# Optimization experiments

Measured on AMD Instinct MI355X. Metric: run time of the kernel, lower is better.

The kernel has to match this reference:

```python
import jax, jax.numpy as jnp
import numpy as np

HIDDEN = 1024
HEADS = 16
HEAD_DIM = HIDDEN // HEADS
FF = 4 * HIDDEN
B, S = 2, 2048


def _linear_params(key, out_dim, in_dim):
    kw, kb = jax.random.split(key)
    bound = 1.0 / np.sqrt(in_dim)
    W = jax.random.uniform(kw, (out_dim, in_dim), jnp.float32, -bound, bound)
    b = jax.random.uniform(kb, (out_dim,), jnp.float32, -bound, bound)
    return W, b


def setup_inputs() -> dict:
    key = jax.random.key(0)
    ks = jax.random.split(key, 8)
    x = jax.random.normal(ks[0], (B, S, HIDDEN), jnp.float32)
    attention_mask = jnp.ones((B, S), jnp.float32)
    Wq, bq = _linear_params(ks[1], HIDDEN, HIDDEN)
    Wk, bk = _linear_params(ks[2], HIDDEN, HIDDEN)
    Wv, bv = _linear_params(ks[3], HIDDEN, HIDDEN)
    Wo, bo = _linear_params(ks[4], HIDDEN, HIDDEN)
    W1, b1 = _linear_params(ks[5], FF, HIDDEN)
    W2, b2 = _linear_params(ks[6], HIDDEN, FF)
    g1 = jnp.ones((HIDDEN,), jnp.float32); be1 = jnp.zeros((HIDDEN,), jnp.float32)
    g2 = jnp.ones((HIDDEN,), jnp.float32); be2 = jnp.zeros((HIDDEN,), jnp.float32)
    return dict(x=x, attention_mask=attention_mask,
                Wq=Wq, bq=bq, Wk=Wk, bk=bk, Wv=Wv, bv=bv, Wo=Wo, bo=bo,
                W1=W1, b1=b1, W2=W2, b2=b2,
                g1=g1, be1=be1, g2=g2, be2=be2)


def _layer_norm(x, g, b, eps=1e-5):
    mu = jnp.mean(x, axis=-1, keepdims=True)
    var = jnp.mean(jnp.square(x - mu), axis=-1, keepdims=True)
    return (x - mu) * jax.lax.rsqrt(var + eps) * g + b


def reference(x, attention_mask, Wq, bq, Wk, bk, Wv, bv, Wo, bo,
              W1, b1, W2, b2, g1, be1, g2, be2):
    # Dropout is identity (eval mode / deterministic reference).
    residual = x
    h = _layer_norm(x, g1, be1)
    # [B,S,H] -> [B,nH,S,dh]
    def heads(t):
        return t.reshape(B, S, HEADS, HEAD_DIM).transpose(0, 2, 1, 3)
    q = heads(h @ Wq.T + bq)
    k = heads(h @ Wk.T + bk)
    v = heads(h @ Wv.T + bv)
    scores = jnp.einsum('bhqd,bhkd->bhqk', q, k) / np.sqrt(HEAD_DIM).astype(np.float32)
    scores = scores + (attention_mask[:, None, None, :] - 1.0) * 10000.0
    attn = jax.nn.softmax(scores, axis=-1)
    ctx = jnp.einsum('bhqk,bhkd->bhqd', attn, v)
    ctx = ctx.transpose(0, 2, 1, 3).reshape(B, S, HIDDEN)
    attn_out = ctx @ Wo.T + bo
    x = residual + attn_out
    residual = x
    h = _layer_norm(x, g2, be2)
    h = jax.nn.gelu(h @ W1.T + b1, approximate=False)
    h = h @ W2.T + b2
    return residual + h
```

## Files before the change

kernel.cpp:

```cpp
#include <hip/hip_runtime.h>
#include <hip/hip_bf16.h>
#include <math.h>

typedef __bf16 bf16;
typedef __bf16 bf16x4v __attribute__((ext_vector_type(4)));
typedef __bf16 bf16x8 __attribute__((ext_vector_type(8)));
typedef float  f32x4  __attribute__((ext_vector_type(4)));

#define HIDDEN 1024
#define TOKENS 4096
#define FFDIM  4096
#define SEQ    2048
#define NHEAD  16

#define LOG2E 1.44269504088896340736f

__device__ __forceinline__ void async_copy16(bf16* lds, const bf16* g)
{
    __builtin_amdgcn_global_load_lds(
        (__attribute__((address_space(1))) void*)g,
        (__attribute__((address_space(3))) void*)lds,
        16, 0, 0);
}

__global__ __launch_bounds__(256) void cvt_kernel(const float* __restrict__ in,
                                                  bf16* __restrict__ out, int n)
{
    int i = (blockIdx.x * 256 + threadIdx.x) * 4;
    if (i >= n) return;
    float4 v = *(const float4*)&in[i];
    bf16x4v o = { (bf16)v.x, (bf16)v.y, (bf16)v.z, (bf16)v.w };
    *(bf16x4v*)&out[i] = o;
}

__global__ __launch_bounds__(256) void cvt4_kernel(const float* __restrict__ s0,
    const float* __restrict__ s1, const float* __restrict__ s2, const float* __restrict__ s3,
    bf16* __restrict__ out)
{
    const int M1 = 1 << 20;
    int i = (blockIdx.x * 256 + threadIdx.x) * 4;
    int sel = i >> 20;
    const float* src = (sel == 0) ? s0 : (sel == 1) ? s1 : (sel == 2) ? s2 : s3;
    float4 v = *(const float4*)&src[i & (M1 - 1)];
    bf16x4v o = { (bf16)v.x, (bf16)v.y, (bf16)v.z, (bf16)v.w };
    *(bf16x4v*)&out[i] = o;
}

__global__ __launch_bounds__(256) void concat_bias_kernel(const float* __restrict__ bq,
    const float* __restrict__ bk, const float* __restrict__ bv, float* __restrict__ o)
{
    int i = blockIdx.x * 256 + threadIdx.x;
    float v = (i < 1024) ? bq[i] : (i < 2048 ? bk[i - 1024] : bv[i - 2048]);
    o[i] = v;
}

__global__ __launch_bounds__(256) void ln_kernel(const float* __restrict__ in,
    const float* __restrict__ g, const float* __restrict__ be, bf16* __restrict__ out)
{
    int row = blockIdx.x;
    int tid = threadIdx.x;
    const float* x = in + (size_t)row * HIDDEN;
    int i0 = tid * 4;
    float4 v = *(const float4*)&x[i0];
    float s  = v.x + v.y + v.z + v.w;
    float s2 = v.x*v.x + v.y*v.y + v.z*v.z + v.w*v.w;
    #pragma unroll
    for (int off = 32; off > 0; off >>= 1) { s += __shfl_xor(s, off); s2 += __shfl_xor(s2, off); }
    __shared__ float red[2][4];
    int wave = tid >> 6;
    if ((tid & 63) == 0) { red[0][wave] = s; red[1][wave] = s2; }
    __syncthreads();
    float ts  = red[0][0] + red[0][1] + red[0][2] + red[0][3];
    float ts2 = red[1][0] + red[1][1] + red[1][2] + red[1][3];
    float mu   = ts  * (1.0f / HIDDEN);
    float var  = ts2 * (1.0f / HIDDEN) - mu * mu;
    float rstd = rsqrtf(var + 1e-5f);
    float4 gg = *(const float4*)&g[i0];
    float4 bb = *(const float4*)&be[i0];
    bf16x4v o;
    o[0] = (bf16)((v.x - mu) * rstd * gg.x + bb.x);
    o[1] = (bf16)((v.y - mu) * rstd * gg.y + bb.y);
    o[2] = (bf16)((v.z - mu) * rstd * gg.z + bb.z);
    o[3] = (bf16)((v.w - mu) * rstd * gg.w + bb.w);
    *(bf16x4v*)&out[(size_t)row * HIDDEN + i0] = o;
}

template<int BM, int EPI, typename OT>
__global__ __launch_bounds__(256) void gemm_bt(const bf16* __restrict__ A, const bf16* __restrict__ Bt,
    const float* __restrict__ bias, const float* __restrict__ res, OT* __restrict__ C,
    int M, int N, int K)
{
    constexpr int MT = BM / 32;
    __shared__ bf16 As[BM * 64];
    __shared__ bf16 Bs[128 * 64];
    int tid  = threadIdx.x;
    int wave = tid >> 6, lane = tid & 63;
    int lm = lane & 15, quad = lane >> 4;
    int m0 = blockIdx.x * BM, n0 = blockIdx.y * 128;
    int wm = (wave >> 1) * (MT * 16), wn = (wave & 1) * 64;
    int r8 = lane >> 3, c8 = lane & 7;
    int gsw = (c8 ^ (r8 & 7)) * 8;
    f32x4 acc[MT][4] = {};
    for (int k0 = 0; k0 < K; k0 += 64) {
        #pragma unroll
        for (int ch = wave; ch < BM / 8; ch += 4)
            async_copy16(As + ch * 512, &A[(size_t)(m0 + ch * 8 + r8) * K + k0 + gsw]);
        #pragma unroll
        for (int ch = wave; ch < 16; ch += 4)
            async_copy16(Bs + ch * 512, &Bt[(size_t)(n0 + ch * 8 + r8) * K + k0 + gsw]);
        __syncthreads();
        bf16x8 af[MT][2], bfr[4][2];
        #pragma unroll
        for (int ks = 0; ks < 2; ks++) {
            int co = ((ks * 4 + quad) ^ (lm & 7)) * 8;
            #pragma unroll
            for (int t = 0; t < MT; t++) af[t][ks]  = *(const bf16x8*)&As[(wm + t * 16 + lm) * 64 + co];
            #pragma unroll
            for (int t = 0; t < 4; t++)  bfr[t][ks] = *(const bf16x8*)&Bs[(wn + t * 16 + lm) * 64 + co];
        }
        #pragma unroll
        for (int mt = 0; mt < MT; mt++)
            #pragma unroll
            for (int nt = 0; nt < 4; nt++)
                #pragma unroll
                for (int ks = 0; ks < 2; ks++)
                    acc[mt][nt] = __builtin_amdgcn_mfma_f32_16x16x32_bf16(af[mt][ks], bfr[nt][ks], acc[mt][nt], 0, 0, 0);
        __syncthreads();
    }
    #pragma unroll
    for (int mt = 0; mt < MT; mt++) {
        #pragma unroll
        for (int nt = 0; nt < 4; nt++) {
            int col = n0 + wn + nt * 16 + lm;
            float bv = bias[col];
            #pragma unroll
            for (int r = 0; r < 4; r++) {
                int row = m0 + wm + mt * 16 + quad * 4 + r;
                float vv = acc[mt][nt][r] + bv;
                if (EPI == 1) vv = 0.5f * vv * (1.0f + erff(vv * 0.70710678118654752f));
                if (EPI == 2) vv += res[(size_t)row * N + col];
                C[(size_t)row * N + col] = (OT)vv;
            }
        }
    }
}

__global__ __launch_bounds__(256) void gemm_qkv(const bf16* __restrict__ A, const bf16* __restrict__ W,
    const float* __restrict__ bias, bf16* __restrict__ qb, bf16* __restrict__ kb, bf16* __restrict__ vt)
{
    constexpr int K = HIDDEN;
    __shared__ bf16 As[128 * 64];
    __shared__ bf16 Bs[128 * 64];
    int tid  = threadIdx.x;
    int wave = tid >> 6, lane = tid & 63;
    int lm = lane & 15, quad = lane >> 4;
    int m0 = blockIdx.x * 128, n0 = blockIdx.y * 128;
    int wm = (wave >> 1) * 64, wn = (wave & 1) * 64;
    int r8 = lane >> 3, c8 = lane & 7;
    int gsw = (c8 ^ (r8 & 7)) * 8;
    f32x4 acc[4][4] = {};
    for (int k0 = 0; k0 < K; k0 += 64) {
        #pragma unroll
        for (int ch = wave; ch < 16; ch += 4) {
            async_copy16(As + ch * 512, &A[(size_t)(m0 + ch * 8 + r8) * K + k0 + gsw]);
            async_copy16(Bs + ch * 512, &W[(size_t)(n0 + ch * 8 + r8) * K + k0 + gsw]);
        }
        __syncthreads();
        bf16x8 af[4][2], bfr[4][2];
        #pragma unroll
        for (int ks = 0; ks < 2; ks++) {
            int co = ((ks * 4 + quad) ^ (lm & 7)) * 8;
            #pragma unroll
            for (int t = 0; t < 4; t++) {
                af[t][ks]  = *(const bf16x8*)&As[(wm + t * 16 + lm) * 64 + co];
                bfr[t][ks] = *(const bf16x8*)&Bs[(wn + t * 16 + lm) * 64 + co];
            }
        }
        #pragma unroll
        for (int mt = 0; mt < 4; mt++)
            #pragma unroll
            for (int nt = 0; nt < 4; nt++)
                #pragma unroll
                for (int ks = 0; ks < 2; ks++)
                    acc[mt][nt] = __builtin_amdgcn_mfma_f32_16x16x32_bf16(af[mt][ks], bfr[nt][ks], acc[mt][nt], 0, 0, 0);
        __syncthreads();
    }
    int region = n0 >> 10;
    #pragma unroll
    for (int mt = 0; mt < 4; mt++) {
        #pragma unroll
        for (int nt = 0; nt < 4; nt++) {
            int col = n0 + wn + nt * 16 + lm;
            float bv = bias[col];
            int cl = col & 1023;
            #pragma unroll
            for (int r = 0; r < 4; r++) {
                int row = m0 + wm + mt * 16 + quad * 4 + r;
                float vv = acc[mt][nt][r] + bv;
                if (region == 0)      qb[(size_t)row * HIDDEN + cl] = (bf16)vv;
                else if (region == 1) kb[(size_t)row * HIDDEN + cl] = (bf16)vv;
                else {
                    int h = cl >> 6, d = cl & 63;
                    int b = row >> 11, s = row & 2047;
                    vt[(((size_t)(b * NHEAD + h)) * 64 + d) * SEQ + s] = (bf16)vv;
                }
            }
        }
    }
}

__global__ __launch_bounds__(256) void attn_kernel(const bf16* __restrict__ Q, const bf16* __restrict__ K,
    const bf16* __restrict__ Vt, const float* __restrict__ mask, bf16* __restrict__ O)
{
    __shared__ bf16 Ks[64 * 64];
    __shared__ bf16 Vs[64 * 64];
    __shared__ bf16 Ps[4][16 * 72];
    int tid = threadIdx.x, wave = tid >> 6, lane = tid & 63;
    int lm = lane & 15, quad = lane >> 4;
    int bh = blockIdx.y, b = bh >> 4, h = bh & 15;
    int q0 = blockIdx.x * 64 + wave * 16;
    const size_t base  = ((size_t)b * SEQ) * HIDDEN + h * 64;
    const size_t vbase = (size_t)bh * 64 * SEQ;
    int srow8 = lane >> 3, spos = lane & 7;
    bf16x8 qf[2];
    #pragma unroll
    for (int ks = 0; ks < 2; ks++)
        qf[ks] = *(const bf16x8*)&Q[base + (size_t)(q0 + lm) * HIDDEN + ks * 32 + quad * 8];
    f32x4 o[4] = {};
    float lsum = 0.0f;
    const float c0 = 0.125f * LOG2E;
    const float cmk = 10000.0f * LOG2E;
    const float coff = -(cmk + 16.0f);
    bf16* pw = &Ps[wave][0];
    for (int kt = 0; kt < SEQ; kt += 64) {
        __syncthreads();
        #pragma unroll
        for (int ch = wave; ch < 8; ch += 4) {
            int r = ch * 8 + srow8;
            int gc = spos ^ (r & 7);
            async_copy16(Ks + ch * 512, &K [base  + (size_t)(kt + r) * HIDDEN + gc * 8]);
            async_copy16(Vs + ch * 512, &Vt[vbase + (size_t)r * SEQ + kt + gc * 8]);
        }
        __syncthreads();
        f32x4 st[4] = {};
        #pragma unroll
        for (int nt = 0; nt < 4; nt++) {
            #pragma unroll
            for (int ks = 0; ks < 2; ks++) {
                bf16x8 kf = *(const bf16x8*)&Ks[(nt * 16 + lm) * 64 + (((ks * 4 + quad) ^ (lm & 7)) * 8)];
                st[nt] = __builtin_amdgcn_mfma_f32_16x16x32_bf16(kf, qf[ks], st[nt], 0, 0, 0);
            }
        }
        #pragma unroll
        for (int nt = 0; nt < 4; nt++) {
            float4 mv = *(const float4*)&mask[b * SEQ + kt + nt * 16 + quad * 4];
            float p0 = exp2f(st[nt][0] * c0 + (mv.x * cmk + coff));
            float p1 = exp2f(st[nt][1] * c0 + (mv.y * cmk + coff));
            float p2 = exp2f(st[nt][2] * c0 + (mv.z * cmk + coff));
            float p3 = exp2f(st[nt][3] * c0 + (mv.w * cmk + coff));
            lsum += (p0 + p1) + (p2 + p3);
            bf16x4v pk = { (bf16)p0, (bf16)p1, (bf16)p2, (bf16)p3 };
            *(bf16x4v*)&pw[lm * 72 + nt * 16 + quad * 4] = pk;
        }
        bf16x8 pf[2];
        #pragma unroll
        for (int ks = 0; ks < 2; ks++)
            pf[ks] = *(const bf16x8*)&pw[lm * 72 + ks * 32 + quad * 8];
        #pragma unroll
        for (int dt = 0; dt < 4; dt++) {
            #pragma unroll
            for (int ks = 0; ks < 2; ks++) {
                bf16x8 vf = *(const bf16x8*)&Vs[(dt * 16 + lm) * 64 + (((ks * 4 + quad) ^ (lm & 7)) * 8)];
                o[dt] = __builtin_amdgcn_mfma_f32_16x16x32_bf16(pf[ks], vf, o[dt], 0, 0, 0);
            }
        }
    }
    lsum += __shfl_xor(lsum, 16);
    lsum += __shfl_xor(lsum, 32);
    #pragma unroll
    for (int r = 0; r < 4; r++) {
        float lr = __shfl(lsum, quad * 4 + r);
        float inv = 1.0f / lr;
        #pragma unroll
        for (int dt = 0; dt < 4; dt++) {
            float val = o[dt][r] * inv;
            O[base + (size_t)(q0 + quad * 4 + r) * HIDDEN + dt * 16 + lm] = (bf16)val;
        }
    }
}

extern "C" void kernel_launch(void* const* d_in, const int* in_sizes, int n_in,
                              void* d_out, int out_size, void* d_ws, size_t ws_size,
                              hipStream_t stream)
{
    (void)in_sizes; (void)n_in; (void)out_size; (void)ws_size;
    const float* x    = (const float*)d_in[0];
    const float* mask = (const float*)d_in[1];
    const float* Wq   = (const float*)d_in[2];
    const float* bq   = (const float*)d_in[3];
    const float* Wk   = (const float*)d_in[4];
    const float* bk   = (const float*)d_in[5];
    const float* Wv   = (const float*)d_in[6];
    const float* bv   = (const float*)d_in[7];
    const float* Wo   = (const float*)d_in[8];
    const float* bo   = (const float*)d_in[9];
    const float* W1   = (const float*)d_in[10];
    const float* b1   = (const float*)d_in[11];
    const float* W2   = (const float*)d_in[12];
    const float* b2   = (const float*)d_in[13];
    const float* g1   = (const float*)d_in[14];
    const float* be1  = (const float*)d_in[15];
    const float* g2   = (const float*)d_in[16];
    const float* be2  = (const float*)d_in[17];
    float* out = (float*)d_out;

    const size_t M1 = 1024u * 1024u;
    bf16* ws    = (bf16*)d_ws;
    bf16* Wqkv_b = ws;
    bf16* Wo_b  = ws + 3 * M1;
    bf16* W1_b  = ws + 4 * M1;
    bf16* W2_b  = ws + 8 * M1;
    bf16* qb    = ws + 12 * M1;
    bf16* kb    = ws + 16 * M1;
    bf16* vt    = ws + 20 * M1;
    bf16* cx    = ws + 24 * M1;
    bf16* h     = ws + 28 * M1;
    bf16* ffb   = ws + 12 * M1;
    float* biasqkv = (float*)(ws + 24 * M1);

    cvt4_kernel<<<dim3(4096), 256, 0, stream>>>(Wq, Wk, Wv, Wo, Wqkv_b);
    cvt_kernel<<<dim3(4 * M1 / 1024), 256, 0, stream>>>(W1, W1_b, 4 * M1);
    cvt_kernel<<<dim3(4 * M1 / 1024), 256, 0, stream>>>(W2, W2_b, 4 * M1);
    concat_bias_kernel<<<dim3(12), 256, 0, stream>>>(bq, bk, bv, biasqkv);

    ln_kernel<<<dim3(TOKENS), 256, 0, stream>>>(x, g1, be1, h);
    gemm_qkv<<<dim3(32, 24), 256, 0, stream>>>(h, Wqkv_b, biasqkv, qb, kb, vt);
    attn_kernel<<<dim3(SEQ / 64, 32), 256, 0, stream>>>(qb, kb, vt, mask, cx);
    gemm_bt<64, 2, float><<<dim3(64, 8), 256, 0, stream>>>(cx, Wo_b, bo, x, out, TOKENS, HIDDEN, HIDDEN);
    ln_kernel<<<dim3(TOKENS), 256, 0, stream>>>(out, g2, be2, h);
    gemm_bt<128, 1, bf16><<<dim3(32, 32), 256, 0, stream>>>(h, W1_b, b1, nullptr, ffb, TOKENS, FFDIM, HIDDEN);
    gemm_bt<64, 2, float><<<dim3(64, 8), 256, 0, stream>>>(ffb, W2_b, b2, out, out, TOKENS, HIDDEN, FFDIM);
}
```

Before: 397.3 us.

## Double-buffer LDS in GEMMs and attention, shrink tiles, sum softmax via MFMA

Adds double-buffered LDS staging to all GEMM kernels and the attention kernel, so the async global-to-LDS load of the next K tile overlaps the MFMA work on the current one. This drops one barrier per iteration. It also shrinks the QKV and FFN1 GEMM M-tile from 128 to 64, which doubles grid size and lowers per-thread accumulators. In attention, the per-row softmax denominator is now accumulated with an extra MFMA against a ones vector instead of scalar adds and shuffles, and exp2f is replaced by the hardware exp2 intrinsic. The costs are more LDS per block, possibly lower occupancy, and less data reuse from the smaller GEMM tiles.

```diff
diff --git a/kernel.cpp b/kernel.cpp
--- a/kernel.cpp
+++ b/kernel.cpp
@@ -85,50 +85,57 @@
     *(bf16x4v*)&out[(size_t)row * HIDDEN + i0] = o;
 }
 
-template<int BM, int EPI, typename OT>
+template<int EPI, typename OT>
 __global__ __launch_bounds__(256) void gemm_bt(const bf16* __restrict__ A, const bf16* __restrict__ Bt,
     const float* __restrict__ bias, const float* __restrict__ res, OT* __restrict__ C,
     int M, int N, int K)
 {
-    constexpr int MT = BM / 32;
-    __shared__ bf16 As[BM * 64];
-    __shared__ bf16 Bs[128 * 64];
+    __shared__ bf16 As[2][64 * 64];
+    __shared__ bf16 Bs[2][128 * 64];
     int tid  = threadIdx.x;
     int wave = tid >> 6, lane = tid & 63;
     int lm = lane & 15, quad = lane >> 4;
-    int m0 = blockIdx.x * BM, n0 = blockIdx.y * 128;
-    int wm = (wave >> 1) * (MT * 16), wn = (wave & 1) * 64;
+    int m0 = blockIdx.x * 64, n0 = blockIdx.y * 128;
+    int wm = (wave >> 1) * 32, wn = (wave & 1) * 64;
     int r8 = lane >> 3, c8 = lane & 7;
     int gsw = (c8 ^ (r8 & 7)) * 8;
-    f32x4 acc[MT][4] = {};
-    for (int k0 = 0; k0 < K; k0 += 64) {
-        #pragma unroll
-        for (int ch = wave; ch < BM / 8; ch += 4)
-            async_copy16(As + ch * 512, &A[(size_t)(m0 + ch * 8 + r8) * K + k0 + gsw]);
+    const bf16* Ab = A  + (size_t)(m0 + r8) * K + gsw;
+    const bf16* Bb = Bt + (size_t)(n0 + r8) * K + gsw;
+    int ntiles = K >> 6;
+    auto stage = [&](int buf, int k0) {
+        #pragma unroll
+        for (int ch = wave; ch < 8; ch += 4)
+            async_copy16(&As[buf][ch * 512], Ab + (size_t)(ch * 8) * K + k0);
         #pragma unroll
         for (int ch = wave; ch < 16; ch += 4)
-            async_copy16(Bs + ch * 512, &Bt[(size_t)(n0 + ch * 8 + r8) * K + k0 + gsw]);
+            async_copy16(&Bs[buf][ch * 512], Bb + (size_t)(ch * 8) * K + k0);
+    };
+    stage(0, 0);
+    f32x4 acc[2][4] = {};
+    for (int t = 0; t < ntiles; t++) {
         __syncthreads();
-        bf16x8 af[MT][2], bfr[4][2];
+        if (t + 1 < ntiles) stage((t + 1) & 1, (t + 1) << 6);
+        const bf16* as = As[t & 1];
+        const bf16* bs = Bs[t & 1];
+        bf16x8 af[2][2], bfr[4][2];
         #pragma unroll
         for (int ks = 0; ks < 2; ks++) {
             int co = ((ks * 4 + quad) ^ (lm & 7)) * 8;
             #pragma unroll
-            for (int t = 0; t < MT; t++) af[t][ks]  = *(const bf16x8*)&As[(wm + t * 16 + lm) * 64 + co];
-            #pragma unroll
-            for (int t = 0; t < 4; t++)  bfr[t][ks] = *(const bf16x8*)&Bs[(wn + t * 16 + lm) * 64 + co];
-        }
-        #pragma unroll
-        for (int mt = 0; mt < MT; mt++)
+            for (int u = 0; u < 2; u++) af[u][ks]  = *(const bf16x8*)&as[(wm + u * 16 + lm) * 64 + co];
+            #pragma unroll
+            for (int u = 0; u < 4; u++) bfr[u][ks] = *(const bf16x8*)&bs[(wn + u * 16 + lm) * 64 + co];
+        }
+        #pragma unroll
+        for (int mt = 0; mt < 2; mt++)
             #pragma unroll
             for (int nt = 0; nt < 4; nt++)
                 #pragma unroll
                 for (int ks = 0; ks < 2; ks++)
                     acc[mt][nt] = __builtin_amdgcn_mfma_f32_16x16x32_bf16(af[mt][ks], bfr[nt][ks], acc[mt][nt], 0, 0, 0);
-        __syncthreads();
-    }
-    #pragma unroll
-    for (int mt = 0; mt < MT; mt++) {
+    }
+    #pragma unroll
+    for (int mt = 0; mt < 2; mt++) {
         #pragma unroll
         for (int nt = 0; nt < 4; nt++) {
             int col = n0 + wn + nt * 16 + lm;
@@ -149,45 +156,53 @@
     const float* __restrict__ bias, bf16* __restrict__ qb, bf16* __restrict__ kb, bf16* __restrict__ vt)
 {
     constexpr int K = HIDDEN;
-    __shared__ bf16 As[128 * 64];
-    __shared__ bf16 Bs[128 * 64];
+    constexpr int N = 3072;
+    __shared__ bf16 As[2][64 * 64];
+    __shared__ bf16 Bs[2][128 * 64];
     int tid  = threadIdx.x;
     int wave = tid >> 6, lane = tid & 63;
     int lm = lane & 15, quad = lane >> 4;
-    int m0 = blockIdx.x * 128, n0 = blockIdx.y * 128;
-    int wm = (wave >> 1) * 64, wn = (wave & 1) * 64;
+    int m0 = blockIdx.x * 64, n0 = blockIdx.y * 128;
+    int wm = (wave >> 1) * 32, wn = (wave & 1) * 64;
     int r8 = lane >> 3, c8 = lane & 7;
     int gsw = (c8 ^ (r8 & 7)) * 8;
-    f32x4 acc[4][4] = {};
-    for (int k0 = 0; k0 < K; k0 += 64) {
-        #pragma unroll
-        for (int ch = wave; ch < 16; ch += 4) {
-            async_copy16(As + ch * 512, &A[(size_t)(m0 + ch * 8 + r8) * K + k0 + gsw]);
-            async_copy16(Bs + ch * 512, &W[(size_t)(n0 + ch * 8 + r8) * K + k0 + gsw]);
-        }
+    const bf16* Ab = A + (size_t)(m0 + r8) * K + gsw;
+    const bf16* Bb = W + (size_t)(n0 + r8) * K + gsw;
+    auto stage = [&](int buf, int k0) {
+        #pragma unroll
+        for (int ch = wave; ch < 8; ch += 4)
+            async_copy16(&As[buf][ch * 512], Ab + (size_t)(ch * 8) * K + k0);
+        #pragma unroll
+        for (int ch = wave; ch < 16; ch += 4)
+            async_copy16(&Bs[buf][ch * 512], Bb + (size_t)(ch * 8) * K + k0);
+    };
+    stage(0, 0);
+    f32x4 acc[2][4] = {};
+    for (int t = 0; t < K / 64; t++) {
         __syncthreads();
-        bf16x8 af[4][2], bfr[4][2];
+        if (t + 1 < K / 64) stage((t + 1) & 1, (t + 1) << 6);
+        const bf16* as = As[t & 1];
+        const bf16* bs = Bs[t & 1];
+        bf16x8 af[2][2], bfr[4][2];
         #pragma unroll
         for (int ks = 0; ks < 2; ks++) {
             int co = ((ks * 4 + quad) ^ (lm & 7)) * 8;
             #pragma unroll
-            for (int t = 0; t < 4; t++) {
-                af[t][ks]  = *(const bf16x8*)&As[(wm + t * 16 + lm) * 64 + co];
-                bfr[t][ks] = *(const bf16x8*)&Bs[(wn + t * 16 + lm) * 64 + co];
-            }
-        }
-        #pragma unroll
-        for (int mt = 0; mt < 4; mt++)
+            for (int u = 0; u < 2; u++) af[u][ks]  = *(const bf16x8*)&as[(wm + u * 16 + lm) * 64 + co];
+            #pragma unroll
+            for (int u = 0; u < 4; u++) bfr[u][ks] = *(const bf16x8*)&bs[(wn + u * 16 + lm) * 64 + co];
+        }
+        #pragma unroll
+        for (int mt = 0; mt < 2; mt++)
             #pragma unroll
             for (int nt = 0; nt < 4; nt++)
                 #pragma unroll
                 for (int ks = 0; ks < 2; ks++)
                     acc[mt][nt] = __builtin_amdgcn_mfma_f32_16x16x32_bf16(af[mt][ks], bfr[nt][ks], acc[mt][nt], 0, 0, 0);
-        __syncthreads();
     }
     int region = n0 >> 10;
     #pragma unroll
-    for (int mt = 0; mt < 4; mt++) {
+    for (int mt = 0; mt < 2; mt++) {
         #pragma unroll
         for (int nt = 0; nt < 4; nt++) {
             int col = n0 + wn + nt * 16 + lm;
@@ -207,13 +222,14 @@
             }
         }
     }
+    (void)N;
 }
 
 __global__ __launch_bounds__(256) void attn_kernel(const bf16* __restrict__ Q, const bf16* __restrict__ K,
     const bf16* __restrict__ Vt, const float* __restrict__ mask, bf16* __restrict__ O)
 {
-    __shared__ bf16 Ks[64 * 64];
-    __shared__ bf16 Vs[64 * 64];
+    __shared__ bf16 Ks[2][64 * 64];
+    __shared__ bf16 Vs[2][64 * 64];
     __shared__ bf16 Ps[4][16 * 72];
     int tid = threadIdx.x, wave = tid >> 6, lane = tid & 63;
     int lm = lane & 15, quad = lane >> 4;
@@ -226,39 +242,47 @@
     #pragma unroll
     for (int ks = 0; ks < 2; ks++)
         qf[ks] = *(const bf16x8*)&Q[base + (size_t)(q0 + lm) * HIDDEN + ks * 32 + quad * 8];
+    bf16x8 onesf;
+    #pragma unroll
+    for (int i = 0; i < 8; i++) onesf[i] = (bf16)1.0f;
     f32x4 o[4] = {};
-    float lsum = 0.0f;
+    f32x4 lacc = {};
     const float c0 = 0.125f * LOG2E;
     const float cmk = 10000.0f * LOG2E;
     const float coff = -(cmk + 16.0f);
     bf16* pw = &Ps[wave][0];
-    for (int kt = 0; kt < SEQ; kt += 64) {
-        __syncthreads();
+    auto stage = [&](int buf, int kt) {
         #pragma unroll
         for (int ch = wave; ch < 8; ch += 4) {
             int r = ch * 8 + srow8;
             int gc = spos ^ (r & 7);
-            async_copy16(Ks + ch * 512, &K [base  + (size_t)(kt + r) * HIDDEN + gc * 8]);
-            async_copy16(Vs + ch * 512, &Vt[vbase + (size_t)r * SEQ + kt + gc * 8]);
-        }
+            async_copy16(&Ks[buf][ch * 512], &K [base  + (size_t)(kt + r) * HIDDEN + gc * 8]);
+            async_copy16(&Vs[buf][ch * 512], &Vt[vbase + (size_t)r * SEQ + kt + gc * 8]);
+        }
+    };
+    stage(0, 0);
+    for (int ti = 0; ti < SEQ / 64; ti++) {
         __syncthreads();
+        if (ti + 1 < SEQ / 64) stage((ti + 1) & 1, (ti + 1) * 64);
+        const bf16* ksb = Ks[ti & 1];
+        const bf16* vsb = Vs[ti & 1];
+        int kt = ti * 64;
         f32x4 st[4] = {};
         #pragma unroll
         for (int nt = 0; nt < 4; nt++) {
             #pragma unroll
             for (int ks = 0; ks < 2; ks++) {
-                bf16x8 kf = *(const bf16x8*)&Ks[(nt * 16 + lm) * 64 + (((ks * 4 + quad) ^ (lm & 7)) * 8)];
+                bf16x8 kf = *(const bf16x8*)&ksb[(nt * 16 + lm) * 64 + (((ks * 4 + quad) ^ (lm & 7)) * 8)];
                 st[nt] = __builtin_amdgcn_mfma_f32_16x16x32_bf16(kf, qf[ks], st[nt], 0, 0, 0);
             }
         }
         #pragma unroll
         for (int nt = 0; nt < 4; nt++) {
             float4 mv = *(const float4*)&mask[b * SEQ + kt + nt * 16 + quad * 4];
-            float p0 = exp2f(st[nt][0] * c0 + (mv.x * cmk + coff));
-            float p1 = exp2f(st[nt][1] * c0 + (mv.y * cmk + coff));
-            float p2 = exp2f(st[nt][2] * c0 + (mv.z * cmk + coff));
-            float p3 = exp2f(st[nt][3] * c0 + (mv.w * cmk + coff));
-            lsum += (p0 + p1) + (p2 + p3);
+            float p0 = __builtin_amdgcn_exp2f(st[nt][0] * c0 + (mv.x * cmk + coff));
+            float p1 = __builtin_amdgcn_exp2f(st[nt][1] * c0 + (mv.y * cmk + coff));
+            float p2 = __builtin_amdgcn_exp2f(st[nt][2] * c0 + (mv.z * cmk + coff));
+            float p3 = __builtin_amdgcn_exp2f(st[nt][3] * c0 + (mv.w * cmk + coff));
             bf16x4v pk = { (bf16)p0, (bf16)p1, (bf16)p2, (bf16)p3 };
             *(bf16x4v*)&pw[lm * 72 + nt * 16 + quad * 4] = pk;
         }
@@ -266,21 +290,20 @@
         #pragma unroll
         for (int ks = 0; ks < 2; ks++)
             pf[ks] = *(const bf16x8*)&pw[lm * 72 + ks * 32 + quad * 8];
+        lacc = __builtin_amdgcn_mfma_f32_16x16x32_bf16(pf[0], onesf, lacc, 0, 0, 0);
+        lacc = __builtin_amdgcn_mfma_f32_16x16x32_bf16(pf[1], onesf, lacc, 0, 0, 0);
         #pragma unroll
         for (int dt = 0; dt < 4; dt++) {
             #pragma unroll
             for (int ks = 0; ks < 2; ks++) {
-                bf16x8 vf = *(const bf16x8*)&Vs[(dt * 16 + lm) * 64 + (((ks * 4 + quad) ^ (lm & 7)) * 8)];
+                bf16x8 vf = *(const bf16x8*)&vsb[(dt * 16 + lm) * 64 + (((ks * 4 + quad) ^ (lm & 7)) * 8)];
                 o[dt] = __builtin_amdgcn_mfma_f32_16x16x32_bf16(pf[ks], vf, o[dt], 0, 0, 0);
             }
         }
     }
-    lsum += __shfl_xor(lsum, 16);
-    lsum += __shfl_xor(lsum, 32);
     #pragma unroll
     for (int r = 0; r < 4; r++) {
-        float lr = __shfl(lsum, quad * 4 + r);
-        float inv = 1.0f / lr;
+        float inv = 1.0f / lacc[r];
         #pragma unroll
         for (int dt = 0; dt < 4; dt++) {
             float val = o[dt][r] * inv;
@@ -334,10 +357,10 @@
     concat_bias_kernel<<<dim3(12), 256, 0, stream>>>(bq, bk, bv, biasqkv);
 
     ln_kernel<<<dim3(TOKENS), 256, 0, stream>>>(x, g1, be1, h);
-    gemm_qkv<<<dim3(32, 24), 256, 0, stream>>>(h, Wqkv_b, biasqkv, qb, kb, vt);
+    gemm_qkv<<<dim3(64, 24), 256, 0, stream>>>(h, Wqkv_b, biasqkv, qb, kb, vt);
     attn_kernel<<<dim3(SEQ / 64, 32), 256, 0, stream>>>(qb, kb, vt, mask, cx);
-    gemm_bt<64, 2, float><<<dim3(64, 8), 256, 0, stream>>>(cx, Wo_b, bo, x, out, TOKENS, HIDDEN, HIDDEN);
+    gemm_bt<2, float><<<dim3(64, 8), 256, 0, stream>>>(cx, Wo_b, bo, x, out, TOKENS, HIDDEN, HIDDEN);
     ln_kernel<<<dim3(TOKENS), 256, 0, stream>>>(out, g2, be2, h);
-    gemm_bt<128, 1, bf16><<<dim3(32, 32), 256, 0, stream>>>(h, W1_b, b1, nullptr, ffb, TOKENS, FFDIM, HIDDEN);
-    gemm_bt<64, 2, float><<<dim3(64, 8), 256, 0, stream>>>(ffb, W2_b, b2, out, out, TOKENS, HIDDEN, FFDIM);
-}
+    gemm_bt<1, bf16><<<dim3(64, 32), 256, 0, stream>>>(h, W1_b, b1, nullptr, ffb, TOKENS, FFDIM, HIDDEN);
+    gemm_bt<2, float><<<dim3(64, 8), 256, 0, stream>>>(ffb, W2_b, b2, out, out, TOKENS, HIDDEN, FFDIM);
+}
```

New measurement: 412.2 us. 3.8% more time.
